# Optimization experiments

Hardware: AMD Instinct MI355X
Metric: run time of the kernel (lower is better)

Reference implementation:

```python
import jax, jax.numpy as jnp
import numpy as np

LR = 0.01
EPS = 1e-8
D, H, O, N = 1024, 256, 64, 1024


def _normalize(W, b):
    # L2 (Frobenius) normalize weights and biases, clamped at EPS
    wn = jnp.maximum(jnp.sqrt(jnp.sum(W * W)), EPS)
    bn = jnp.maximum(jnp.sqrt(jnp.sum(b * b)), EPS)
    return W / wn, b / bn


def _step(carry, xt):
    W1, b1, W2, b2, W3, b3 = carry
    x, t = xt
    # forward pass (3-layer sigmoid MLP, softmax over -a3 as in original)
    a1 = jax.nn.sigmoid(x @ W1 + b1)
    a2 = jax.nn.sigmoid(a1 @ W2 + b2)
    a3 = jax.nn.sigmoid(a2 @ W3 + b3)
    out = jax.nn.softmax(-a3)
    # manual backprop deltas
    d3 = (t - out) * a3 * (1.0 - a3)
    o2 = (W3 @ d3) * a2 * (1.0 - a2)
    o1 = (W2 @ o2) * a1 * (1.0 - a1)
    # SGD update (note: original subtracts the delta, matching .sub_)
    W3 = W3 - LR * jnp.outer(a2, d3)
    b3 = b3 - LR * d3
    W2 = W2 - LR * jnp.outer(a1, o2)
    b2 = b2 - LR * o2
    W1 = W1 - LR * jnp.outer(x, o1)
    b1 = b1 - LR * o1
    # L2 normalize each layer's weights/biases
    W1, b1 = _normalize(W1, b1)
    W2, b2 = _normalize(W2, b2)
    W3, b3 = _normalize(W3, b3)
    return (W1, b1, W2, b2, W3, b3), None


def setup_inputs() -> dict:
    key = jax.random.key(0)
    k = jax.random.split(key, 5)
    return {
        "training_data": jax.random.normal(k[0], (N, D), jnp.float32),
        "training_targets": jax.random.uniform(k[1], (N, O), dtype=jnp.float32),
        "weights1": jax.random.normal(k[2], (D, H), jnp.float32) * 0.01,
        "biases1": jnp.zeros((H,), jnp.float32),
        "weights2": jax.random.normal(k[3], (H, H), jnp.float32) * 0.01,
        "biases2": jnp.zeros((H,), jnp.float32),
        "weights3": jax.random.normal(k[4], (H, O), jnp.float32) * 0.01,
        "biases3": jnp.zeros((O,), jnp.float32),
    }


def reference(training_data, training_targets, weights1, biases1, weights2, biases2, weights3, biases3):
    carry0 = (weights1, biases1, weights2, biases2, weights3, biases3)
    carry, _ = jax.lax.scan(_step, carry0, (training_data, training_targets))
    W1, b1, W2, b2, W3, b3 = carry
    return (W1, W2, W3)
```

## Files before the change

kernel.cpp:

```cpp
#include <hip/hip_runtime.h>
#include <math.h>


#define LRC  0.01f
#define EPSV 1e-8f

typedef float f32x8 __attribute__((ext_vector_type(8)));

#define SMEM_FLOATS 36384
#define SMEM_BYTES  (SMEM_FLOATS * 4)

#define ROWS16(OP)                                                            \
  OP(0) OP(1) OP(2) OP(3) OP(4) OP(5) OP(6) OP(7)                             \
  OP(8) OP(9) OP(10) OP(11) OP(12) OP(13) OP(14) OP(15)

__device__ __forceinline__ float hsum8(f32x8 v) {
  return ((v.s0 + v.s1) + (v.s2 + v.s3)) + ((v.s4 + v.s5) + (v.s6 + v.s7));
}

template <int CTRL>
__device__ __forceinline__ float dpp_add(float v) {
  const int s = __builtin_amdgcn_update_dpp(0, __builtin_bit_cast(int, v),
                                            CTRL, 0xf, 0xf, true);
  return v + __builtin_bit_cast(float, s);
}

__device__ __forceinline__ float dpp_allred64(float v) {
  v = dpp_add<0x111>(v);
  v = dpp_add<0x112>(v);
  v = dpp_add<0x114>(v);
  v = dpp_add<0x118>(v);
  v = dpp_add<0x142>(v);
  v = dpp_add<0x143>(v);
  return __builtin_bit_cast(float,
      __builtin_amdgcn_readlane(__builtin_bit_cast(int, v), 63));
}

__device__ __forceinline__ float wave_allred(float v) {
#pragma unroll
  for (int off = 32; off > 0; off >>= 1) v += __shfl_xor(v, off);
  return v;
}

#define FMA16(c, a, b)                                                        \
  c[0][0] += a.x * b.x; c[0][1] += a.x * b.y; c[0][2] += a.x * b.z; c[0][3] += a.x * b.w; \
  c[1][0] += a.y * b.x; c[1][1] += a.y * b.y; c[1][2] += a.y * b.z; c[1][3] += a.y * b.w; \
  c[2][0] += a.z * b.x; c[2][1] += a.z * b.y; c[2][2] += a.z * b.z; c[2][3] += a.z * b.w; \
  c[3][0] += a.w * b.x; c[3][1] += a.w * b.y; c[3][2] += a.w * b.z; c[3][3] += a.w * b.w;

__global__ __launch_bounds__(256) void k_gram(const float* __restrict__ X,
                                              float* __restrict__ G) {
  const int bi = blockIdx.y, bj = blockIdx.x;
  if (bj > bi) return;
  __shared__ float Xa[32][68];
  __shared__ float Xb[32][68];
  const int tid = threadIdx.x;
  const int tx = tid & 15, ty = tid >> 4;
  float c[4][4] = {};
  for (int k0 = 0; k0 < 1024; k0 += 32) {
    __syncthreads();
    {
      const int row = tid >> 2, kk = (tid & 3) * 8;
      const float* pa = X + (bi * 64 + row) * 1024 + k0 + kk;
      const float4 a0 = *(const float4*)pa;
      const float4 a1 = *(const float4*)(pa + 4);
      Xa[kk + 0][row] = a0.x; Xa[kk + 1][row] = a0.y;
      Xa[kk + 2][row] = a0.z; Xa[kk + 3][row] = a0.w;
      Xa[kk + 4][row] = a1.x; Xa[kk + 5][row] = a1.y;
      Xa[kk + 6][row] = a1.z; Xa[kk + 7][row] = a1.w;
      const float* pb = X + (bj * 64 + row) * 1024 + k0 + kk;
      const float4 b0 = *(const float4*)pb;
      const float4 b1 = *(const float4*)(pb + 4);
      Xb[kk + 0][row] = b0.x; Xb[kk + 1][row] = b0.y;
      Xb[kk + 2][row] = b0.z; Xb[kk + 3][row] = b0.w;
      Xb[kk + 4][row] = b1.x; Xb[kk + 5][row] = b1.y;
      Xb[kk + 6][row] = b1.z; Xb[kk + 7][row] = b1.w;
    }
    __syncthreads();
#pragma unroll
    for (int kk = 0; kk < 32; kk++) {
      const float4 a = *(const float4*)&Xa[kk][ty * 4];
      const float4 b = *(const float4*)&Xb[kk][tx * 4];
      FMA16(c, a, b)
    }
  }
#pragma unroll
  for (int ii = 0; ii < 4; ii++) {
    *(float4*)(G + (bi * 64 + ty * 4 + ii) * 1024 + bj * 64 + tx * 4) =
        make_float4(c[ii][0], c[ii][1], c[ii][2], c[ii][3]);
  }
}

__global__ __launch_bounds__(256) void k_z10(const float* __restrict__ X,
                                             const float* __restrict__ W1g,
                                             float* __restrict__ Z10) {
  const int bi = blockIdx.y, bj = blockIdx.x;
  __shared__ float At[32][68];
  __shared__ float Bt[32][68];
  const int tid = threadIdx.x;
  const int tx = tid & 15, ty = tid >> 4;
  float c[4][4] = {};
  for (int k0 = 0; k0 < 1024; k0 += 32) {
    __syncthreads();
    {
      const int row = tid >> 2, kk = (tid & 3) * 8;
      const float* pa = X + (bi * 64 + row) * 1024 + k0 + kk;
      const float4 a0 = *(const float4*)pa;
      const float4 a1 = *(const float4*)(pa + 4);
      At[kk + 0][row] = a0.x; At[kk + 1][row] = a0.y;
      At[kk + 2][row] = a0.z; At[kk + 3][row] = a0.w;
      At[kk + 4][row] = a1.x; At[kk + 5][row] = a1.y;
      At[kk + 6][row] = a1.z; At[kk + 7][row] = a1.w;
      const int kr = tid >> 3, j8 = (tid & 7) * 8;
      const float* pb = W1g + (k0 + kr) * 256 + bj * 64 + j8;
      *(float4*)&Bt[kr][j8]     = *(const float4*)pb;
      *(float4*)&Bt[kr][j8 + 4] = *(const float4*)(pb + 4);
    }
    __syncthreads();
#pragma unroll
    for (int kk = 0; kk < 32; kk++) {
      const float4 a = *(const float4*)&At[kk][ty * 4];
      const float4 b = *(const float4*)&Bt[kk][tx * 4];
      FMA16(c, a, b)
    }
  }
#pragma unroll
  for (int ii = 0; ii < 4; ii++) {
    *(float4*)(Z10 + (bi * 64 + ty * 4 + ii) * 256 + bj * 64 + tx * 4) =
        make_float4(c[ii][0], c[ii][1], c[ii][2], c[ii][3]);
  }
}

__global__ __launch_bounds__(256) void k_w1out(
    const float* __restrict__ X, const float* __restrict__ o1g,
    const float* __restrict__ cg, const float* __restrict__ W1g,
    const float* __restrict__ sclg, float* __restrict__ outW1) {
  const int bi = blockIdx.y, bj = blockIdx.x;
  __shared__ float At[32][68];
  __shared__ float Bt[32][68];
  const int tid = threadIdx.x;
  const int tx = tid & 15, ty = tid >> 4;
  float c[4][4] = {};
  for (int k0 = 0; k0 < 1024; k0 += 32) {
    __syncthreads();
    {
      const int kr = tid >> 3, m8 = (tid & 7) * 8;
      const float* pa = X + (k0 + kr) * 1024 + bi * 64 + m8;
      *(float4*)&At[kr][m8]     = *(const float4*)pa;
      *(float4*)&At[kr][m8 + 4] = *(const float4*)(pa + 4);
      const float cs = cg[k0 + kr];
      const float* pb = o1g + (k0 + kr) * 256 + bj * 64 + m8;
      float4 b0 = *(const float4*)pb;
      float4 b1 = *(const float4*)(pb + 4);
      b0.x *= cs; b0.y *= cs; b0.z *= cs; b0.w *= cs;
      b1.x *= cs; b1.y *= cs; b1.z *= cs; b1.w *= cs;
      *(float4*)&Bt[kr][m8]     = b0;
      *(float4*)&Bt[kr][m8 + 4] = b1;
    }
    __syncthreads();
#pragma unroll
    for (int kk = 0; kk < 32; kk++) {
      const float4 a = *(const float4*)&At[kk][ty * 4];
      const float4 b = *(const float4*)&Bt[kk][tx * 4];
      FMA16(c, a, b)
    }
  }
  const float s1f = sclg[0];
#pragma unroll
  for (int ii = 0; ii < 4; ii++) {
    const int row = bi * 64 + ty * 4 + ii;
    const float4 w = *(const float4*)(W1g + row * 256 + bj * 64 + tx * 4);
    *(float4*)(outW1 + row * 256 + bj * 64 + tx * 4) =
        make_float4(s1f * (w.x + c[ii][0]), s1f * (w.y + c[ii][1]),
                    s1f * (w.z + c[ii][2]), s1f * (w.w + c[ii][3]));
  }
}

__device__ __forceinline__ float block_reduce8(float v, float* tmp, int tid) {
  v = wave_allred(v);
  __syncthreads();
  if ((tid & 63) == 0) tmp[tid >> 6] = v;
  __syncthreads();
  float s = 0.f;
#pragma unroll
  for (int w = 0; w < 8; w++) s += tmp[w];
  __syncthreads();
  return s;
}

__global__ __launch_bounds__(512, 1) void k2_seq(
    const float* __restrict__ Tg, const float* __restrict__ W1g,
    const float* __restrict__ b1g, const float* __restrict__ W2g,
    const float* __restrict__ b2g, const float* __restrict__ W3g,
    const float* __restrict__ b3g, const float* __restrict__ G,
    const float* __restrict__ Z10, float* __restrict__ o1g,
    float* __restrict__ cg, float* __restrict__ sclg,
    float* __restrict__ outW2, float* __restrict__ outW3) {
  extern __shared__ float sm[];
  float* const zo   = sm;
  float* const Gb   = sm + 17408;
  float* const scr  = sm + 21504;
  float* const Tb   = sm + 29952;
  float* const a1v  = sm + 34048;
  float* const z1v  = sm + 34560;
  float* const z2v  = sm + 34816;
  float* const a2v  = sm + 35072;
  float* const o2v  = sm + 35328;
  float* const b1ps = sm + 35584;
  float* const b2ps = sm + 35840;
  float* const d3v  = sm + 36096;
  float* const b3ps = sm + 36160;
  float* const ch   = sm + 36224;
  float* const dpart= sm + 36288;
  float* const sca  = sm + 36336;
  float* const cpre = sm + 36352;

  const int tid = threadIdx.x;
  const int lane = tid & 63;
  const int w = tid >> 6;
  const int p = tid >> 5;
  const int q = tid & 31;

  f32x8 W2_0, W2_1, W2_2, W2_3, W2_4, W2_5, W2_6, W2_7,
        W2_8, W2_9, W2_10, W2_11, W2_12, W2_13, W2_14, W2_15;
  float W3x_0, W3x_1, W3x_2, W3x_3, W3x_4, W3x_5, W3x_6, W3x_7,
        W3x_8, W3x_9, W3x_10, W3x_11, W3x_12, W3x_13, W3x_14, W3x_15;
  float W3y_0, W3y_1, W3y_2, W3y_3, W3y_4, W3y_5, W3y_6, W3y_7,
        W3y_8, W3y_9, W3y_10, W3y_11, W3y_12, W3y_13, W3y_14, W3y_15;

#define INIT_ROW(i)                                                           \
  { const int row = p * 16 + i;                                               \
    W2_##i  = *(const f32x8*)(W2g + row * 256 + q * 8);                       \
    W3x_##i = W3g[row * 64 + q * 2];                                          \
    W3y_##i = W3g[row * 64 + q * 2 + 1]; }
  ROWS16(INIT_ROW)

  if (tid < 256) { b1ps[tid] = b1g[tid]; b2ps[tid] = b2g[tid]; }
  if (tid < 64) b3ps[tid] = b3g[tid];
  if (tid == 0) {
    sca[0] = 1.f; sca[1] = 1.f; sca[2] = 1.f; sca[3] = 1.f;
    sca[4] = 1.f; sca[5] = 1.f; sca[6] = 0.f; sca[7] = 0.f;
  }

  float acc1 = 0.f;
  for (int i = tid; i < 65536; i += 512) {
    const float4 v = ((const float4*)W1g)[i];
    acc1 += v.x * v.x + v.y * v.y + v.z * v.z + v.w * v.w;
  }
  const float n1init = block_reduce8(acc1, scr, tid);
  float acc2 = 0.f;
#define N2_ROW(i) { f32x8 t = W2_##i * W2_##i; acc2 += hsum8(t); }
  ROWS16(N2_ROW)
  const float n2init = block_reduce8(acc2, scr, tid);
  float acc3 = 0.f;
#define N3_ROW(i) acc3 += W3x_##i * W3x_##i + W3y_##i * W3y_##i;
  ROWS16(N3_ROW)
  const float n3init = block_reduce8(acc3, scr, tid);

  float s1 = 1.f, s2 = 1.f, s3 = 1.f;
  double n1d = (double)n1init;
  float n2 = n2init, n3 = n3init;
  __syncthreads();

  for (int b = 0; b < 16; b++) {
    const int bs = b * 64;
    {
      f32x8 pacc0 = {0.f, 0.f, 0.f, 0.f, 0.f, 0.f, 0.f, 0.f};
      f32x8 pacc1 = pacc0, pacc2 = pacc0, pacc3 = pacc0;
      for (int c0 = 0; c0 < bs; c0 += 32) {
        __syncthreads();
        if (tid < 32) cpre[tid] = cg[c0 + tid];
        {
          const int row = tid >> 3, k4 = (tid & 7) * 4;
          const float4 gv = *(const float4*)(G + (bs + row) * 1024 + c0 + k4);
          Gb[row * 33 + k4 + 0] = gv.x; Gb[row * 33 + k4 + 1] = gv.y;
          Gb[row * 33 + k4 + 2] = gv.z; Gb[row * 33 + k4 + 3] = gv.w;
        }
#pragma unroll
        for (int u = 0; u < 4; u++) {
          const int fi = tid + u * 512;
          ((float4*)scr)[fi] = ((const float4*)(o1g + c0 * 256))[fi];
        }
        __syncthreads();
#pragma unroll 2
        for (int ss = 0; ss < 32; ss++) {
          const float cs = cpre[ss];
          const f32x8 o8 = *(const f32x8*)(scr + ss * 256 + q * 8);
          pacc0 += (Gb[(p * 4 + 0) * 33 + ss] * cs) * o8;
          pacc1 += (Gb[(p * 4 + 1) * 33 + ss] * cs) * o8;
          pacc2 += (Gb[(p * 4 + 2) * 33 + ss] * cs) * o8;
          pacc3 += (Gb[(p * 4 + 3) * 33 + ss] * cs) * o8;
        }
      }
      __syncthreads();
#define ZSTORE(rr)                                                            \
      { const int row = p * 4 + rr;                                           \
        *(f32x8*)(zo + row * 272 + q * 8) =                                   \
            *(const f32x8*)(Z10 + (bs + row) * 256 + q * 8) + pacc##rr; }
      ZSTORE(0) ZSTORE(1) ZSTORE(2) ZSTORE(3)
#pragma unroll
      for (int u = 0; u < 2; u++) {
        const int fi = tid + u * 512;
        const int row = fi >> 4, c4 = fi & 15;
        *(float4*)(Gb + row * 64 + c4 * 4) =
            *(const float4*)(G + (bs + row) * 1024 + bs + c4 * 4);
      }
      ((float4*)Tb)[tid]       = ((const float4*)(Tg + bs * 64))[tid];
      ((float4*)Tb)[tid + 512] = ((const float4*)(Tg + bs * 64))[tid + 512];
      __syncthreads();
    }

    for (int l = 0; l < 64; l++) {
      const int t = bs + l;
      const int cur = (t & 1) * 256, prv = 256 - cur;
      const float s1c = sca[0], rb1c = sca[1], s2c = sca[2],
                  rb2c = sca[3], s3c = sca[4], rb3c = sca[5];

      if (t > 0) {
        const float cw2 = sca[6], cw3 = sca[7];
        const f32x8 o8s = cw2 * (*(const f32x8*)&o2v[q * 8]);
        const float d0s = cw3 * d3v[q * 2], d1s = cw3 * d3v[q * 2 + 1];
#define UPD_ROW(i)                                                            \
        { const float a1o = a1v[prv + p * 16 + i];                            \
          W2_##i += a1o * o8s;                                                \
          const float a2o = a2v[p * 16 + i];                                  \
          W3x_##i += a2o * d0s; W3y_##i += a2o * d1s; }
        ROWS16(UPD_ROW)
      }
      {
        const int jp = tid >> 2, quarter = tid & 3;
        float ax = 0.f, ay = 0.f;
        for (int lp = quarter; lp < l; lp += 4) {
          const float gcs = ch[lp] * Gb[l * 64 + lp];
          const float2 zr = *(const float2*)&zo[lp * 272 + 2 * jp];
          ax += gcs * zr.x; ay += gcs * zr.y;
        }
        ax = dpp_add<0xB1>(ax); ax = dpp_add<0x4E>(ax);
        ay = dpp_add<0xB1>(ay); ay = dpp_add<0x4E>(ay);
        const float2 zop = *(const float2*)&zo[l * 272 + 2 * jp];
        const float2 b1q = *(const float2*)&b1ps[2 * jp];
        const float z1u0 = zop.x + ax, z1u1 = zop.y + ay;
        const float a1x0 = 1.f / (1.f + expf(-(s1c * z1u0 + rb1c * b1q.x)));
        const float a1x1 = 1.f / (1.f + expf(-(s1c * z1u1 + rb1c * b1q.y)));
        if (quarter == 0) {
          *(float2*)&z1v[2 * jp] = make_float2(z1u0, z1u1);
          *(float2*)&a1v[cur + 2 * jp] = make_float2(a1x0, a1x1);
        }
        const float v3 = dpp_allred64(
            quarter == 0 ? a1x0 * a1x0 + a1x1 * a1x1 : 0.f);
        if (lane == 0) dpart[36 + w] = v3;
      }
      __syncthreads();
      {
        f32x8 acc = {0.f, 0.f, 0.f, 0.f, 0.f, 0.f, 0.f, 0.f};
#define B1_ROW(i) acc += a1v[cur + p * 16 + i] * W2_##i;
        ROWS16(B1_ROW)
        *(f32x8*)&scr[p * 264 + q * 8] = acc;
      }
      __syncthreads();
      if (tid < 256) {
        float s = 0.f;
#pragma unroll
        for (int pp = 0; pp < 16; pp++) s += scr[pp * 264 + tid];
        const float z2p = s2c * s;
        z2v[tid] = z2p;
        a2v[tid] = 1.f / (1.f + expf(-(z2p + rb2c * b2ps[tid])));
      }
      __syncthreads();
      {
        float c0a = 0.f, c1a = 0.f;
#define C1_ROW(i)                                                             \
        { const float a2x = a2v[p * 16 + i];                                  \
          c0a += a2x * W3x_##i; c1a += a2x * W3y_##i; }
        ROWS16(C1_ROW)
        scr[(q * 2 + 0) * 17 + p] = c0a;
        scr[(q * 2 + 1) * 17 + p] = c1a;
      }
      __syncthreads();
      if (tid < 64) {
        float s = 0.f;
#pragma unroll
        for (int pp = 0; pp < 16; pp++) s += scr[tid * 17 + pp];
        const float z3p = s3c * s;
        const float a3 = 1.f / (1.f + expf(-(z3p + rb3c * b3ps[tid])));
        const float e = expf(-a3);
        const float tot = dpp_allred64(e);
        const float outv = e / tot;
        const float d3 = (Tb[l * 64 + tid] - outv) * a3 * (1.f - a3);
        d3v[tid] = d3;
        const float b3n = rb3c * b3ps[tid] - LRC * d3;
        b3ps[tid] = b3n;
        const float v5 = dpp_allred64(z3p * d3);
        const float v7 = dpp_allred64(d3 * d3);
        const float v10 = dpp_allred64(b3n * b3n);
        if (tid == 0) { dpart[32] = v5; dpart[33] = v7; dpart[34] = v10; }
      }
      __syncthreads();
      {
        const float d0 = d3v[q * 2 + 0], d1 = d3v[q * 2 + 1];
#define E1_ROW(i) scr[(p * 16 + i) * 33 + q] = W3x_##i * d0 + W3y_##i * d1;
        ROWS16(E1_ROW)
      }
      __syncthreads();
      if (tid < 256) {
        float s = 0.f;
#pragma unroll
        for (int qq = 0; qq < 32; qq++) s += scr[tid * 33 + qq];
        const float a2x = a2v[tid];
        const float o2 = s3c * s * a2x * (1.f - a2x);
        o2v[tid] = o2;
        const float b2n = rb2c * b2ps[tid] - LRC * o2;
        b2ps[tid] = b2n;
        const float v2 = dpp_allred64(z2v[tid] * o2);
        const float v4 = dpp_allred64(o2 * o2);
        const float v6 = dpp_allred64(a2x * a2x);
        const float v9 = dpp_allred64(b2n * b2n);
        if ((tid & 63) == 0) {
          dpart[16 + w] = v2; dpart[20 + w] = v4;
          dpart[24 + w] = v6; dpart[28 + w] = v9;
        }
      }
      __syncthreads();
      {
        const f32x8 ov8 = *(const f32x8*)&o2v[q * 8];
#define F1_ROW(i)                                                             \
        { f32x8 tmp = W2_##i * ov8; scr[(p * 16 + i) * 33 + q] = hsum8(tmp); }
        ROWS16(F1_ROW)
      }
      if (w == 7) {
        const float dts3 = ((dpart[36] + dpart[37]) + (dpart[38] + dpart[39]))
                         + ((dpart[40] + dpart[41]) + (dpart[42] + dpart[43]));
        const float dts2 = (dpart[16] + dpart[17]) + (dpart[18] + dpart[19]);
        const float dts4 = (dpart[20] + dpart[21]) + (dpart[22] + dpart[23]);
        const float dts6 = (dpart[24] + dpart[25]) + (dpart[26] + dpart[27]);
        const float dts9 = (dpart[28] + dpart[29]) + (dpart[30] + dpart[31]);
        const float dts5 = dpart[32], dts7 = dpart[33], dts10 = dpart[34];
        const float n2p = n2 - 2.f * LRC * dts2 + LRC * LRC * dts3 * dts4;
        const float r2s = 1.f / fmaxf(sqrtf(n2p), EPSV);
        n2 = n2p * r2s * r2s;
        const float cw2n = -LRC / s2;
        s2 = s2 * r2s;
        const float n3p = n3 - 2.f * LRC * dts5 + LRC * LRC * dts6 * dts7;
        const float r3s = 1.f / fmaxf(sqrtf(n3p), EPSV);
        n3 = n3p * r3s * r3s;
        const float cw3n = -LRC / s3;
        s3 = s3 * r3s;
        if (lane == 0) {
          sca[2] = s2;
          sca[3] = 1.f / fmaxf(sqrtf(dts9), EPSV);
          sca[4] = s3;
          sca[5] = 1.f / fmaxf(sqrtf(dts10), EPSV);
          sca[6] = cw2n;
          sca[7] = cw3n;
        }
      }
      __syncthreads();
      if (tid < 256) {
        float s = 0.f;
#pragma unroll
        for (int qq = 0; qq < 32; qq++) s += scr[tid * 33 + qq];
        const float a1x = a1v[cur + tid];
        const float o1x = s2c * s * a1x * (1.f - a1x);
        zo[l * 272 + tid] = o1x;
        const float b1n = rb1c * b1ps[tid] - LRC * o1x;
        b1ps[tid] = b1n;
        const float v0 = dpp_allred64(z1v[tid] * o1x);
        const float v1 = dpp_allred64(o1x * o1x);
        const float v8 = dpp_allred64(b1n * b1n);
        if ((tid & 63) == 0) {
          dpart[0 + w] = v0; dpart[4 + w] = v1; dpart[12 + w] = v8;
        }
      }
      __syncthreads();
      if (tid < 64) {
        const float dts0 = (dpart[0] + dpart[1]) + (dpart[2] + dpart[3]);
        const float dts1 = (dpart[4] + dpart[5]) + (dpart[6] + dpart[7]);
        const float dts8 = (dpart[12] + dpart[13]) + (dpart[14] + dpart[15]);
        const float c1 = -LRC / s1;
        const double gtt = (double)Gb[l * 64 + l];
        n1d = n1d + 2.0 * (double)c1 * (double)dts0 +
              (double)c1 * (double)c1 * gtt * (double)dts1;
        const double w1n = (double)s1 * sqrt(n1d);
        s1 = (float)((double)s1 / fmax(w1n, (double)EPSV));
        if (tid == 0) {
          ch[l] = c1;
          sca[0] = s1;
          sca[1] = 1.f / fmaxf(sqrtf(dts8), EPSV);
        }
      }
      __syncthreads();
    }

    {
#pragma unroll
      for (int u = 0; u < 4; u++) {
        const int chunk = tid + u * 512;
        const int row = chunk >> 5, c8 = chunk & 31;
        *(f32x8*)(o1g + (bs + row) * 256 + c8 * 8) =
            *(const f32x8*)(zo + row * 272 + c8 * 8);
      }
      if (tid < 64) cg[bs + tid] = ch[tid];
    }
  }

  {
    const float cw2 = sca[6], cw3 = sca[7];
    const float s2f = sca[2], s3f = sca[4];
    const f32x8 o8s = cw2 * (*(const f32x8*)&o2v[q * 8]);
    const float d0s = cw3 * d3v[q * 2], d1s = cw3 * d3v[q * 2 + 1];
#define FIN_ROW(i)                                                            \
    { const float a1o = a1v[256 + p * 16 + i];          \
      W2_##i += a1o * o8s;                                                    \
      const float a2o = a2v[p * 16 + i];                                      \
      W3x_##i += a2o * d0s; W3y_##i += a2o * d1s;                             \
      const int row = p * 16 + i;                                             \
      *(f32x8*)(outW2 + row * 256 + q * 8) = s2f * W2_##i;                    \
      outW3[row * 64 + q * 2]     = s3f * W3x_##i;                            \
      outW3[row * 64 + q * 2 + 1] = s3f * W3y_##i; }
    ROWS16(FIN_ROW)
    if (tid == 0) sclg[0] = sca[0];
  }
}

extern "C" void kernel_launch(void* const* d_in, const int* in_sizes, int n_in,
                              void* d_out, int out_size, void* d_ws,
                              size_t ws_size, hipStream_t stream) {
  (void)in_sizes; (void)n_in; (void)out_size; (void)ws_size;
  const float* X   = (const float*)d_in[0];
  const float* Tg  = (const float*)d_in[1];
  const float* W1g = (const float*)d_in[2];
  const float* b1g = (const float*)d_in[3];
  const float* W2g = (const float*)d_in[4];
  const float* b2g = (const float*)d_in[5];
  const float* W3g = (const float*)d_in[6];
  const float* b3g = (const float*)d_in[7];
  float* out = (float*)d_out;
  float* ws  = (float*)d_ws;

  float* G    = ws;
  float* Z10  = G + 1048576;
  float* o1g  = Z10 + 262144;
  float* cg   = o1g + 262144;
  float* sclg = cg + 1024;

  (void)hipFuncSetAttribute((const void*)k2_seq,
                            hipFuncAttributeMaxDynamicSharedMemorySize,
                            SMEM_BYTES);

  k_gram<<<dim3(16, 16), 256, 0, stream>>>(X, G);
  k_z10<<<dim3(4, 16), 256, 0, stream>>>(X, W1g, Z10);
  k2_seq<<<dim3(1), dim3(512), SMEM_BYTES, stream>>>(
      Tg, W1g, b1g, W2g, b2g, W3g, b3g, G, Z10, o1g, cg, sclg,
      out + 262144, out + 327680);
  k_w1out<<<dim3(4, 16), 256, 0, stream>>>(X, o1g, cg, W1g, sclg, out);
}
```

Baseline: 8.963 ms.

## Replicate scalar normalization chain per thread and cut per-step barriers

Drops the shared-memory scalar broadcast. Every thread now recomputes the norm/scale recurrence from partial dot products at the start of the next step, so the single-thread scalar stages and their barriers go away. The W3·d3 and W2·o2 row reductions now use an in-register DPP transpose tree instead of a shared-memory scratch round trip. The layer-3 softmax is computed by all waves, and b3 and the partial sums are double-buffered to avoid races. The aim is fewer __syncthreads per sequential step, at the cost of redundant scalar math in every thread and more register pressure.

```diff
diff --git a/kernel.cpp b/kernel.cpp
--- a/kernel.cpp
+++ b/kernel.cpp
@@ -7,7 +7,7 @@
 
 typedef float f32x8 __attribute__((ext_vector_type(8)));
 
-#define SMEM_FLOATS 36384
+#define SMEM_FLOATS 36456
 #define SMEM_BYTES  (SMEM_FLOATS * 4)
 
 #define ROWS16(OP)                                                            \
@@ -19,12 +19,14 @@
 }
 
 template <int CTRL>
+__device__ __forceinline__ float dpp_mov(float x) {
+  return __builtin_bit_cast(float, __builtin_amdgcn_update_dpp(
+      0, __builtin_bit_cast(int, x), CTRL, 0xf, 0xf, true));
+}
+template <int CTRL>
 __device__ __forceinline__ float dpp_add(float v) {
-  const int s = __builtin_amdgcn_update_dpp(0, __builtin_bit_cast(int, v),
-                                            CTRL, 0xf, 0xf, true);
-  return v + __builtin_bit_cast(float, s);
-}
-
+  return v + dpp_mov<CTRL>(v);
+}
 __device__ __forceinline__ float dpp_allred64(float v) {
   v = dpp_add<0x111>(v);
   v = dpp_add<0x112>(v);
@@ -35,12 +37,37 @@
   return __builtin_bit_cast(float,
       __builtin_amdgcn_readlane(__builtin_bit_cast(int, v), 63));
 }
+__device__ __forceinline__ float dpp_xor4(float x, bool hi) {
+  const float up = dpp_mov<0x104>(x);
+  const float dn = dpp_mov<0x114>(x);
+  return hi ? dn : up;
+}
+__device__ __forceinline__ float dpp_xor8(float x, bool hi) {
+  const float up = dpp_mov<0x108>(x);
+  const float dn = dpp_mov<0x118>(x);
+  return hi ? dn : up;
+}
 
 __device__ __forceinline__ float wave_allred(float v) {
 #pragma unroll
   for (int off = 32; off > 0; off >>= 1) v += __shfl_xor(v, off);
   return v;
 }
+
+#define TSTAGE(XEXPR, BITVAL, N2)                                             \
+  { _Pragma("unroll")                                                         \
+    for (int s = 0; s < N2; s++) {                                            \
+      const float aa = v[2 * s], bb = v[2 * s + 1];                           \
+      const float snd = (BITVAL) ? aa : bb;                                   \
+      const float kp = (BITVAL) ? bb : aa;                                    \
+      v[s] = kp + (XEXPR);                                                    \
+    } }
+#define TREE16()                                                              \
+  TSTAGE(dpp_mov<0xB1>(snd), bt1, 8)                                          \
+  TSTAGE(dpp_mov<0x4E>(snd), bt2, 4)                                          \
+  TSTAGE(dpp_xor4(snd, bt4), bt4, 2)                                          \
+  TSTAGE(dpp_xor8(snd, bt8), bt8, 1)                                          \
+  v[0] += __shfl_xor(v[0], 16);
 
 #define FMA16(c, a, b)                                                        \
   c[0][0] += a.x * b.x; c[0][1] += a.x * b.y; c[0][2] += a.x * b.z; c[0][3] += a.x * b.w; \
@@ -210,16 +237,18 @@
   float* const b2ps = sm + 35840;
   float* const d3v  = sm + 36096;
   float* const b3ps = sm + 36160;
-  float* const ch   = sm + 36224;
-  float* const dpart= sm + 36288;
-  float* const sca  = sm + 36336;
-  float* const cpre = sm + 36352;
+  float* const ch   = sm + 36288;
+  float* const dpart= sm + 36352;
+  float* const cpre = sm + 36424;
 
   const int tid = threadIdx.x;
   const int lane = tid & 63;
   const int w = tid >> 6;
   const int p = tid >> 5;
   const int q = tid & 31;
+  const int gl = lane & 31;
+  const bool bt1 = (lane & 1), bt2 = (lane & 2), bt4 = (lane & 4),
+             bt8 = (lane & 8);
 
   f32x8 W2_0, W2_1, W2_2, W2_3, W2_4, W2_5, W2_6, W2_7,
         W2_8, W2_9, W2_10, W2_11, W2_12, W2_13, W2_14, W2_15;
@@ -237,10 +266,6 @@
 
   if (tid < 256) { b1ps[tid] = b1g[tid]; b2ps[tid] = b2g[tid]; }
   if (tid < 64) b3ps[tid] = b3g[tid];
-  if (tid == 0) {
-    sca[0] = 1.f; sca[1] = 1.f; sca[2] = 1.f; sca[3] = 1.f;
-    sca[4] = 1.f; sca[5] = 1.f; sca[6] = 0.f; sca[7] = 0.f;
-  }
 
   float acc1 = 0.f;
   for (int i = tid; i < 65536; i += 512) {
@@ -258,9 +283,60 @@
   const float n3init = block_reduce8(acc3, scr, tid);
 
   float s1 = 1.f, s2 = 1.f, s3 = 1.f;
+  float rb1 = 1.f, rb2 = 1.f, rb3 = 1.f;
+  float c1r = 0.f, cw2r = 0.f, cw3r = 0.f;
   double n1d = (double)n1init;
   float n2 = n2init, n3 = n3init;
   __syncthreads();
+
+  auto run_chain = [&](const int lidx, const int pv3) {
+    const float4 qa0 = *(const float4*)&dpart[0];
+    const float4 qa1 = *(const float4*)&dpart[4];
+    const float4 qb0 = *(const float4*)&dpart[8];
+    const float4 qb1 = *(const float4*)&dpart[12];
+    const float4 qc0 = *(const float4*)&dpart[16];
+    const float4 qc1 = *(const float4*)&dpart[20];
+    const float4 qd0 = *(const float4*)&dpart[24];
+    const float4 qd1 = *(const float4*)&dpart[28];
+    const float4 qe0 = *(const float4*)&dpart[32];
+    const float4 qe1 = *(const float4*)&dpart[36];
+    const float4 qf0 = *(const float4*)&dpart[40];
+    const float4 qf1 = *(const float4*)&dpart[44];
+    const float4 qg0 = *(const float4*)&dpart[48 + pv3];
+    const float4 qg1 = *(const float4*)&dpart[52 + pv3];
+    const float4 qh  = *(const float4*)&dpart[64];
+    const float4 qi  = *(const float4*)&dpart[68];
+#define SUM8(x0, x1) (((x0.x + x0.y) + (x0.z + x0.w)) +                       \
+                      ((x1.x + x1.y) + (x1.z + x1.w)))
+    const float dts0 = SUM8(qa0, qa1);
+    const float dts1 = SUM8(qb0, qb1);
+    const float dts8 = SUM8(qc0, qc1);
+    const float dts2 = SUM8(qd0, qd1);
+    const float dts4 = SUM8(qe0, qe1);
+    const float dts9 = SUM8(qf0, qf1);
+    const float dts3 = SUM8(qg0, qg1);
+    const float dts5 = qh.x, dts7 = qh.y, dts10 = qh.z;
+    const float dts6 = (qi.x + qi.y) + (qi.z + qi.w);
+    const float c1 = -LRC / s1;
+    c1r = c1; cw2r = -LRC / s2; cw3r = -LRC / s3;
+    const double gtt = (double)Gb[lidx * 65];
+    n1d = n1d + 2.0 * (double)c1 * (double)dts0 +
+          (double)c1 * (double)c1 * gtt * (double)dts1;
+    const double w1n = (double)s1 * sqrt(n1d);
+    s1 = (float)((double)s1 / fmax(w1n, (double)EPSV));
+    rb1 = 1.f / fmaxf(sqrtf(dts8), EPSV);
+    const float n2p = n2 - 2.f * LRC * dts2 + LRC * LRC * dts3 * dts4;
+    const float r2s = 1.f / fmaxf(sqrtf(n2p), EPSV);
+    n2 = n2p * r2s * r2s;
+    s2 = s2 * r2s;
+    rb2 = 1.f / fmaxf(sqrtf(dts9), EPSV);
+    const float n3p = n3 - 2.f * LRC * dts5 + LRC * LRC * dts6 * dts7;
+    const float r3s = 1.f / fmaxf(sqrtf(n3p), EPSV);
+    n3 = n3p * r3s * r3s;
+    s3 = s3 * r3s;
+    rb3 = 1.f / fmaxf(sqrtf(dts10), EPSV);
+    if (tid == 0) ch[lidx] = c1;
+  };
 
   for (int b = 0; b < 16; b++) {
     const int bs = b * 64;
@@ -313,13 +389,11 @@
     for (int l = 0; l < 64; l++) {
       const int t = bs + l;
       const int cur = (t & 1) * 256, prv = 256 - cur;
-      const float s1c = sca[0], rb1c = sca[1], s2c = sca[2],
-                  rb2c = sca[3], s3c = sca[4], rb3c = sca[5];
-
+
+      if (l > 0) run_chain(l - 1, ((t - 1) & 1) * 8);
       if (t > 0) {
-        const float cw2 = sca[6], cw3 = sca[7];
-        const f32x8 o8s = cw2 * (*(const f32x8*)&o2v[q * 8]);
-        const float d0s = cw3 * d3v[q * 2], d1s = cw3 * d3v[q * 2 + 1];
+        const f32x8 o8s = cw2r * (*(const f32x8*)&o2v[q * 8]);
+        const float d0s = cw3r * d3v[q * 2], d1s = cw3r * d3v[q * 2 + 1];
 #define UPD_ROW(i)                                                            \
         { const float a1o = a1v[prv + p * 16 + i];                            \
           W2_##i += a1o * o8s;                                                \
@@ -330,9 +404,14 @@
       {
         const int jp = tid >> 2, quarter = tid & 3;
         float ax = 0.f, ay = 0.f;
-        for (int lp = quarter; lp < l; lp += 4) {
+        for (int lp = quarter; lp < l - 1; lp += 4) {
           const float gcs = ch[lp] * Gb[l * 64 + lp];
           const float2 zr = *(const float2*)&zo[lp * 272 + 2 * jp];
+          ax += gcs * zr.x; ay += gcs * zr.y;
+        }
+        if (l > 0 && ((l - 1) & 3) == quarter) {
+          const float gcs = c1r * Gb[l * 64 + (l - 1)];
+          const float2 zr = *(const float2*)&zo[(l - 1) * 272 + 2 * jp];
           ax += gcs * zr.x; ay += gcs * zr.y;
         }
         ax = dpp_add<0xB1>(ax); ax = dpp_add<0x4E>(ax);
@@ -340,17 +419,18 @@
         const float2 zop = *(const float2*)&zo[l * 272 + 2 * jp];
         const float2 b1q = *(const float2*)&b1ps[2 * jp];
         const float z1u0 = zop.x + ax, z1u1 = zop.y + ay;
-        const float a1x0 = 1.f / (1.f + expf(-(s1c * z1u0 + rb1c * b1q.x)));
-        const float a1x1 = 1.f / (1.f + expf(-(s1c * z1u1 + rb1c * b1q.y)));
+        const float a1x0 = 1.f / (1.f + expf(-(s1 * z1u0 + rb1 * b1q.x)));
+        const float a1x1 = 1.f / (1.f + expf(-(s1 * z1u1 + rb1 * b1q.y)));
         if (quarter == 0) {
           *(float2*)&z1v[2 * jp] = make_float2(z1u0, z1u1);
           *(float2*)&a1v[cur + 2 * jp] = make_float2(a1x0, a1x1);
         }
         const float v3 = dpp_allred64(
             quarter == 0 ? a1x0 * a1x0 + a1x1 * a1x1 : 0.f);
-        if (lane == 0) dpart[36 + w] = v3;
-      }
-      __syncthreads();
+        if (lane == 0) dpart[48 + (t & 1) * 8 + w] = v3;
+      }
+      __syncthreads();
+
       {
         f32x8 acc = {0.f, 0.f, 0.f, 0.f, 0.f, 0.f, 0.f, 0.f};
 #define B1_ROW(i) acc += a1v[cur + p * 16 + i] * W2_##i;
@@ -358,138 +438,108 @@
         *(f32x8*)&scr[p * 264 + q * 8] = acc;
       }
       __syncthreads();
+
       if (tid < 256) {
         float s = 0.f;
 #pragma unroll
         for (int pp = 0; pp < 16; pp++) s += scr[pp * 264 + tid];
-        const float z2p = s2c * s;
+        const float z2p = s2 * s;
         z2v[tid] = z2p;
-        a2v[tid] = 1.f / (1.f + expf(-(z2p + rb2c * b2ps[tid])));
-      }
-      __syncthreads();
+        const float a2x = 1.f / (1.f + expf(-(z2p + rb2 * b2ps[tid])));
+        a2v[tid] = a2x;
+        const float v6w = dpp_allred64(a2x * a2x);
+        if ((tid & 63) == 0) dpart[68 + (tid >> 6)] = v6w;
+      }
+      __syncthreads();
+
       {
         float c0a = 0.f, c1a = 0.f;
 #define C1_ROW(i)                                                             \
         { const float a2x = a2v[p * 16 + i];                                  \
           c0a += a2x * W3x_##i; c1a += a2x * W3y_##i; }
         ROWS16(C1_ROW)
-        scr[(q * 2 + 0) * 17 + p] = c0a;
-        scr[(q * 2 + 1) * 17 + p] = c1a;
-      }
-      __syncthreads();
-      if (tid < 64) {
-        float s = 0.f;
-#pragma unroll
-        for (int pp = 0; pp < 16; pp++) s += scr[tid * 17 + pp];
-        const float z3p = s3c * s;
-        const float a3 = 1.f / (1.f + expf(-(z3p + rb3c * b3ps[tid])));
-        const float e = expf(-a3);
-        const float tot = dpp_allred64(e);
-        const float outv = e / tot;
-        const float d3 = (Tb[l * 64 + tid] - outv) * a3 * (1.f - a3);
-        d3v[tid] = d3;
-        const float b3n = rb3c * b3ps[tid] - LRC * d3;
-        b3ps[tid] = b3n;
-        const float v5 = dpp_allred64(z3p * d3);
-        const float v7 = dpp_allred64(d3 * d3);
-        const float v10 = dpp_allred64(b3n * b3n);
-        if (tid == 0) { dpart[32] = v5; dpart[33] = v7; dpart[34] = v10; }
-      }
-      __syncthreads();
+        *(float2*)&scr[p * 130 + 2 * q] = make_float2(c0a, c1a);
+      }
+      __syncthreads();
+
       {
-        const float d0 = d3v[q * 2 + 0], d1 = d3v[q * 2 + 1];
-#define E1_ROW(i) scr[(p * 16 + i) * 33 + q] = W3x_##i * d0 + W3y_##i * d1;
-        ROWS16(E1_ROW)
-      }
-      __syncthreads();
-      if (tid < 256) {
-        float s = 0.f;
-#pragma unroll
-        for (int qq = 0; qq < 32; qq++) s += scr[tid * 33 + qq];
-        const float a2x = a2v[tid];
-        const float o2 = s3c * s * a2x * (1.f - a2x);
-        o2v[tid] = o2;
-        const float b2n = rb2c * b2ps[tid] - LRC * o2;
-        b2ps[tid] = b2n;
-        const float v2 = dpp_allred64(z2v[tid] * o2);
-        const float v4 = dpp_allred64(o2 * o2);
-        const float v6 = dpp_allred64(a2x * a2x);
-        const float v9 = dpp_allred64(b2n * b2n);
-        if ((tid & 63) == 0) {
-          dpart[16 + w] = v2; dpart[20 + w] = v4;
-          dpart[24 + w] = v6; dpart[28 + w] = v9;
-        }
-      }
-      __syncthreads();
+        float z30 = 0.f, z31 = 0.f;
+#pragma unroll
+        for (int pp = 0; pp < 16; pp++) {
+          const float2 zz = *(const float2*)&scr[pp * 130 + 2 * q];
+          z30 += zz.x; z31 += zz.y;
+        }
+        const float z3p0 = s3 * z30, z3p1 = s3 * z31;
+        const int pbR = (t & 1) * 64, pbW = 64 - pbR;
+        const float b3o0 = b3ps[pbR + 2 * q], b3o1 = b3ps[pbR + 2 * q + 1];
+        const float a30 = 1.f / (1.f + expf(-(z3p0 + rb3 * b3o0)));
+        const float a31 = 1.f / (1.f + expf(-(z3p1 + rb3 * b3o1)));
+        const float e0 = expf(-a30), e1 = expf(-a31);
+        const float tot2 = dpp_allred64(e0 + e1);
+        const float out0 = (2.f * e0) / tot2, out1 = (2.f * e1) / tot2;
+        const float2 tb = *(const float2*)&Tb[l * 64 + 2 * q];
+        const float d30 = (tb.x - out0) * a30 * (1.f - a30);
+        const float d31 = (tb.y - out1) * a31 * (1.f - a31);
+        const float b3n0 = rb3 * b3o0 - LRC * d30;
+        const float b3n1 = rb3 * b3o1 - LRC * d31;
+        if (tid < 32) {
+          d3v[2 * q] = d30; d3v[2 * q + 1] = d31;
+          b3ps[pbW + 2 * q] = b3n0; b3ps[pbW + 2 * q + 1] = b3n1;
+        }
+        const float v5w = dpp_allred64(z3p0 * d30 + z3p1 * d31);
+        const float v7w = dpp_allred64(d30 * d30 + d31 * d31);
+        const float v10w = dpp_allred64(b3n0 * b3n0 + b3n1 * b3n1);
+        if (tid == 0) {
+          dpart[64] = 0.5f * v5w; dpart[65] = 0.5f * v7w;
+          dpart[66] = 0.5f * v10w;
+        }
+        float v[16];
+#define CE_ROW(i) v[i] = W3x_##i * d30 + W3y_##i * d31;
+        ROWS16(CE_ROW)
+        TREE16()
+        const int r = p * 16 + (gl & 15);
+        const float a2x = a2v[r];
+        const float o2x = s3 * v[0] * a2x * (1.f - a2x);
+        const float z2x = z2v[r];
+        const float b2o = b2ps[r];
+        const float b2n = rb2 * b2o - LRC * o2x;
+        if (gl < 16) { o2v[r] = o2x; b2ps[r] = b2n; }
+        const bool own = gl < 16;
+        const float v2w = dpp_allred64(own ? z2x * o2x : 0.f);
+        const float v4w = dpp_allred64(own ? o2x * o2x : 0.f);
+        const float v9w = dpp_allred64(own ? b2n * b2n : 0.f);
+        if (lane == 0) {
+          dpart[24 + w] = v2w; dpart[32 + w] = v4w; dpart[40 + w] = v9w;
+        }
+      }
+      __syncthreads();
+
       {
         const f32x8 ov8 = *(const f32x8*)&o2v[q * 8];
-#define F1_ROW(i)                                                             \
-        { f32x8 tmp = W2_##i * ov8; scr[(p * 16 + i) * 33 + q] = hsum8(tmp); }
-        ROWS16(F1_ROW)
-      }
-      if (w == 7) {
-        const float dts3 = ((dpart[36] + dpart[37]) + (dpart[38] + dpart[39]))
-                         + ((dpart[40] + dpart[41]) + (dpart[42] + dpart[43]));
-        const float dts2 = (dpart[16] + dpart[17]) + (dpart[18] + dpart[19]);
-        const float dts4 = (dpart[20] + dpart[21]) + (dpart[22] + dpart[23]);
-        const float dts6 = (dpart[24] + dpart[25]) + (dpart[26] + dpart[27]);
-        const float dts9 = (dpart[28] + dpart[29]) + (dpart[30] + dpart[31]);
-        const float dts5 = dpart[32], dts7 = dpart[33], dts10 = dpart[34];
-        const float n2p = n2 - 2.f * LRC * dts2 + LRC * LRC * dts3 * dts4;
-        const float r2s = 1.f / fmaxf(sqrtf(n2p), EPSV);
-        n2 = n2p * r2s * r2s;
-        const float cw2n = -LRC / s2;
-        s2 = s2 * r2s;
-        const float n3p = n3 - 2.f * LRC * dts5 + LRC * LRC * dts6 * dts7;
-        const float r3s = 1.f / fmaxf(sqrtf(n3p), EPSV);
-        n3 = n3p * r3s * r3s;
-        const float cw3n = -LRC / s3;
-        s3 = s3 * r3s;
+        float v[16];
+#define F_ROW(i) { f32x8 tq = W2_##i * ov8; v[i] = hsum8(tq); }
+        ROWS16(F_ROW)
+        TREE16()
+        const int r = p * 16 + (gl & 15);
+        const float a1x = a1v[cur + r];
+        const float o1x = s2 * v[0] * a1x * (1.f - a1x);
+        const float b1o = b1ps[r];
+        const float b1n = rb1 * b1o - LRC * o1x;
+        const float z1x = z1v[r];
+        if (gl < 16) { zo[l * 272 + r] = o1x; b1ps[r] = b1n; }
+        const bool own = gl < 16;
+        const float v0w = dpp_allred64(own ? z1x * o1x : 0.f);
+        const float v1w = dpp_allred64(own ? o1x * o1x : 0.f);
+        const float v8w = dpp_allred64(own ? b1n * b1n : 0.f);
         if (lane == 0) {
-          sca[2] = s2;
-          sca[3] = 1.f / fmaxf(sqrtf(dts9), EPSV);
-          sca[4] = s3;
-          sca[5] = 1.f / fmaxf(sqrtf(dts10), EPSV);
-          sca[6] = cw2n;
-          sca[7] = cw3n;
-        }
-      }
-      __syncthreads();
-      if (tid < 256) {
-        float s = 0.f;
-#pragma unroll
-        for (int qq = 0; qq < 32; qq++) s += scr[tid * 33 + qq];
-        const float a1x = a1v[cur + tid];
-        const float o1x = s2c * s * a1x * (1.f - a1x);
-        zo[l * 272 + tid] = o1x;
-        const float b1n = rb1c * b1ps[tid] - LRC * o1x;
-        b1ps[tid] = b1n;
-        const float v0 = dpp_allred64(z1v[tid] * o1x);
-        const float v1 = dpp_allred64(o1x * o1x);
-        const float v8 = dpp_allred64(b1n * b1n);
-        if ((tid & 63) == 0) {
-          dpart[0 + w] = v0; dpart[4 + w] = v1; dpart[12 + w] = v8;
-        }
-      }
-      __syncthreads();
-      if (tid < 64) {
-        const float dts0 = (dpart[0] + dpart[1]) + (dpart[2] + dpart[3]);
-        const float dts1 = (dpart[4] + dpart[5]) + (dpart[6] + dpart[7]);
-        const float dts8 = (dpart[12] + dpart[13]) + (dpart[14] + dpart[15]);
-        const float c1 = -LRC / s1;
-        const double gtt = (double)Gb[l * 64 + l];
-        n1d = n1d + 2.0 * (double)c1 * (double)dts0 +
-              (double)c1 * (double)c1 * gtt * (double)dts1;
-        const double w1n = (double)s1 * sqrt(n1d);
-        s1 = (float)((double)s1 / fmax(w1n, (double)EPSV));
-        if (tid == 0) {
-          ch[l] = c1;
-          sca[0] = s1;
-          sca[1] = 1.f / fmaxf(sqrtf(dts8), EPSV);
-        }
-      }
-      __syncthreads();
-    }
+          dpart[0 + w] = v0w; dpart[8 + w] = v1w; dpart[16 + w] = v8w;
+        }
+      }
+      __syncthreads();
+    }
+
+    run_chain(63, ((bs + 63) & 1) * 8);
+    __syncthreads();
 
     {
 #pragma unroll
@@ -504,21 +554,19 @@
   }
 
   {
-    const float cw2 = sca[6], cw3 = sca[7];
-    const float s2f = sca[2], s3f = sca[4];
-    const f32x8 o8s = cw2 * (*(const f32x8*)&o2v[q * 8]);
-    const float d0s = cw3 * d3v[q * 2], d1s = cw3 * d3v[q * 2 + 1];
+    const f32x8 o8s = cw2r * (*(const f32x8*)&o2v[q * 8]);
+    const float d0s = cw3r * d3v[q * 2], d1s = cw3r * d3v[q * 2 + 1];
 #define FIN_ROW(i)                                                            \
     { const float a1o = a1v[256 + p * 16 + i];          \
       W2_##i += a1o * o8s;                                                    \
       const float a2o = a2v[p * 16 + i];                                      \
       W3x_##i += a2o * d0s; W3y_##i += a2o * d1s;                             \
       const int row = p * 16 + i;                                             \
-      *(f32x8*)(outW2 + row * 256 + q * 8) = s2f * W2_##i;                    \
-      outW3[row * 64 + q * 2]     = s3f * W3x_##i;                            \
-      outW3[row * 64 + q * 2 + 1] = s3f * W3y_##i; }
+      *(f32x8*)(outW2 + row * 256 + q * 8) = s2 * W2_##i;                     \
+      outW3[row * 64 + q * 2]     = s3 * W3x_##i;                             \
+      outW3[row * 64 + q * 2 + 1] = s3 * W3y_##i; }
     ROWS16(FIN_ROW)
-    if (tid == 0) sclg[0] = sca[0];
+    if (tid == 0) sclg[0] = s1;
   }
 }
 
```

Result: slower. 10.56 ms (+17.8%).

## Defer W2 rank-1 update off critical path and cut per-step barriers

Applied to the files above, without the earlier changes.

The lagged W2 outer-product update now runs in otherwise idle warps during the layer-2/layer-3 reductions. The forward z2 is corrected algebraically with a dot product of the current and previous a1 vectors. The o2 and o1 row reductions are folded into the same phase as their scratch writes, each wave reducing its own rows behind a waitcnt fence, which removes two block-wide barriers per sample. The risk is extra reductions, a changed summation order and a fragile reliance on wave-local ordering of LDS writes.

```diff
diff --git a/kernel.cpp b/kernel.cpp
--- a/kernel.cpp
+++ b/kernel.cpp
@@ -7,7 +7,7 @@
 
 typedef float f32x8 __attribute__((ext_vector_type(8)));
 
-#define SMEM_FLOATS 36384
+#define SMEM_FLOATS 36400
 #define SMEM_BYTES  (SMEM_FLOATS * 4)
 
 #define ROWS16(OP)                                                            \
@@ -40,6 +40,12 @@
 #pragma unroll
   for (int off = 32; off > 0; off >>= 1) v += __shfl_xor(v, off);
   return v;
+}
+
+__device__ __forceinline__ void wave_fence() {
+  __builtin_amdgcn_sched_barrier(0);
+  asm volatile("s_waitcnt lgkmcnt(0)" ::: "memory");
+  __builtin_amdgcn_sched_barrier(0);
 }
 
 #define FMA16(c, a, b)                                                        \
@@ -212,14 +218,15 @@
   float* const b3ps = sm + 36160;
   float* const ch   = sm + 36224;
   float* const dpart= sm + 36288;
-  float* const sca  = sm + 36336;
-  float* const cpre = sm + 36352;
+  float* const sca  = sm + 36360;
+  float* const cpre = sm + 36368;
 
   const int tid = threadIdx.x;
   const int lane = tid & 63;
   const int w = tid >> 6;
   const int p = tid >> 5;
   const int q = tid & 31;
+  const int rown = 32 * w + (lane & 31);
 
   f32x8 W2_0, W2_1, W2_2, W2_3, W2_4, W2_5, W2_6, W2_7,
         W2_8, W2_9, W2_10, W2_11, W2_12, W2_13, W2_14, W2_15;
@@ -235,7 +242,11 @@
     W3y_##i = W3g[row * 64 + q * 2 + 1]; }
   ROWS16(INIT_ROW)
 
-  if (tid < 256) { b1ps[tid] = b1g[tid]; b2ps[tid] = b2g[tid]; }
+  if (tid < 256) {
+    b1ps[tid] = b1g[tid]; b2ps[tid] = b2g[tid];
+    o2v[tid] = 0.f;
+    a1v[tid] = 0.f; a1v[256 + tid] = 0.f;
+  }
   if (tid < 64) b3ps[tid] = b3g[tid];
   if (tid == 0) {
     sca[0] = 1.f; sca[1] = 1.f; sca[2] = 1.f; sca[3] = 1.f;
@@ -313,19 +324,27 @@
     for (int l = 0; l < 64; l++) {
       const int t = bs + l;
       const int cur = (t & 1) * 256, prv = 256 - cur;
-      const float s1c = sca[0], rb1c = sca[1], s2c = sca[2],
-                  rb2c = sca[3], s3c = sca[4], rb3c = sca[5];
+      const float s1c = sca[0], rb1c = sca[1], s2c = sca[2], rb2c = sca[3],
+                  s3c = sca[4], rb3c = sca[5], cw2c = sca[6], cw3c = sca[7];
+
+#define W2_UPD()                                                              \
+      { const f32x8 o8s = cw2c * (*(const f32x8*)&o2v[q * 8]);                \
+        const float* apv = &a1v[prv + p * 16];                                \
+        W2_0  += apv[0]  * o8s; W2_1  += apv[1]  * o8s;                       \
+        W2_2  += apv[2]  * o8s; W2_3  += apv[3]  * o8s;                       \
+        W2_4  += apv[4]  * o8s; W2_5  += apv[5]  * o8s;                       \
+        W2_6  += apv[6]  * o8s; W2_7  += apv[7]  * o8s;                       \
+        W2_8  += apv[8]  * o8s; W2_9  += apv[9]  * o8s;                       \
+        W2_10 += apv[10] * o8s; W2_11 += apv[11] * o8s;                       \
+        W2_12 += apv[12] * o8s; W2_13 += apv[13] * o8s;                       \
+        W2_14 += apv[14] * o8s; W2_15 += apv[15] * o8s; }
 
       if (t > 0) {
-        const float cw2 = sca[6], cw3 = sca[7];
-        const f32x8 o8s = cw2 * (*(const f32x8*)&o2v[q * 8]);
-        const float d0s = cw3 * d3v[q * 2], d1s = cw3 * d3v[q * 2 + 1];
-#define UPD_ROW(i)                                                            \
-        { const float a1o = a1v[prv + p * 16 + i];                            \
-          W2_##i += a1o * o8s;                                                \
-          const float a2o = a2v[p * 16 + i];                                  \
+        const float d0s = cw3c * d3v[q * 2], d1s = cw3c * d3v[q * 2 + 1];
+#define UPD3_ROW(i)                                                           \
+        { const float a2o = a2v[p * 16 + i];                                  \
           W3x_##i += a2o * d0s; W3y_##i += a2o * d1s; }
-        ROWS16(UPD_ROW)
+        ROWS16(UPD3_ROW)
       }
       {
         const int jp = tid >> 2, quarter = tid & 3;
@@ -339,6 +358,7 @@
         ay = dpp_add<0xB1>(ay); ay = dpp_add<0x4E>(ay);
         const float2 zop = *(const float2*)&zo[l * 272 + 2 * jp];
         const float2 b1q = *(const float2*)&b1ps[2 * jp];
+        const float2 ap  = *(const float2*)&a1v[prv + 2 * jp];
         const float z1u0 = zop.x + ax, z1u1 = zop.y + ay;
         const float a1x0 = 1.f / (1.f + expf(-(s1c * z1u0 + rb1c * b1q.x)));
         const float a1x1 = 1.f / (1.f + expf(-(s1c * z1u1 + rb1c * b1q.y)));
@@ -348,9 +368,12 @@
         }
         const float v3 = dpp_allred64(
             quarter == 0 ? a1x0 * a1x0 + a1x1 * a1x1 : 0.f);
-        if (lane == 0) dpart[36 + w] = v3;
-      }
-      __syncthreads();
+        const float vad = dpp_allred64(
+            quarter == 0 ? a1x0 * ap.x + a1x1 * ap.y : 0.f);
+        if (lane == 0) { dpart[48 + w] = v3; dpart[56 + w] = vad; }
+      }
+      __syncthreads();
+
       {
         f32x8 acc = {0.f, 0.f, 0.f, 0.f, 0.f, 0.f, 0.f, 0.f};
 #define B1_ROW(i) acc += a1v[cur + p * 16 + i] * W2_##i;
@@ -358,15 +381,24 @@
         *(f32x8*)&scr[p * 264 + q * 8] = acc;
       }
       __syncthreads();
+
       if (tid < 256) {
         float s = 0.f;
 #pragma unroll
         for (int pp = 0; pp < 16; pp++) s += scr[pp * 264 + tid];
-        const float z2p = s2c * s;
+        const float adot = ((dpart[56] + dpart[57]) + (dpart[58] + dpart[59]))
+                         + ((dpart[60] + dpart[61]) + (dpart[62] + dpart[63]));
+        const float z2p = s2c * (s + cw2c * adot * o2v[tid]);
         z2v[tid] = z2p;
-        a2v[tid] = 1.f / (1.f + expf(-(z2p + rb2c * b2ps[tid])));
-      }
-      __syncthreads();
+        const float a2x = 1.f / (1.f + expf(-(z2p + rb2c * b2ps[tid])));
+        a2v[tid] = a2x;
+        const float v6 = dpp_allred64(a2x * a2x);
+        if ((tid & 63) == 0) dpart[64 + (tid >> 6)] = v6;
+      } else if (t > 0) {
+        W2_UPD()
+      }
+      __syncthreads();
+
       {
         float c0a = 0.f, c1a = 0.f;
 #define C1_ROW(i)                                                             \
@@ -377,64 +409,104 @@
         scr[(q * 2 + 1) * 17 + p] = c1a;
       }
       __syncthreads();
-      if (tid < 64) {
+
+      if (w == 7) {
         float s = 0.f;
 #pragma unroll
-        for (int pp = 0; pp < 16; pp++) s += scr[tid * 17 + pp];
+        for (int pp = 0; pp < 16; pp++) s += scr[lane * 17 + pp];
         const float z3p = s3c * s;
-        const float a3 = 1.f / (1.f + expf(-(z3p + rb3c * b3ps[tid])));
+        const float a3 = 1.f / (1.f + expf(-(z3p + rb3c * b3ps[lane])));
         const float e = expf(-a3);
         const float tot = dpp_allred64(e);
         const float outv = e / tot;
-        const float d3 = (Tb[l * 64 + tid] - outv) * a3 * (1.f - a3);
-        d3v[tid] = d3;
-        const float b3n = rb3c * b3ps[tid] - LRC * d3;
-        b3ps[tid] = b3n;
+        const float d3 = (Tb[l * 64 + lane] - outv) * a3 * (1.f - a3);
+        d3v[lane] = d3;
+        const float b3n = rb3c * b3ps[lane] - LRC * d3;
+        b3ps[lane] = b3n;
         const float v5 = dpp_allred64(z3p * d3);
         const float v7 = dpp_allred64(d3 * d3);
         const float v10 = dpp_allred64(b3n * b3n);
-        if (tid == 0) { dpart[32] = v5; dpart[33] = v7; dpart[34] = v10; }
-      }
-      __syncthreads();
+        if (lane == 0) { dpart[68] = v5; dpart[69] = v7; dpart[70] = v10; }
+      } else if (w < 4 && t > 0) {
+        W2_UPD()
+      }
+      __syncthreads();
+
       {
         const float d0 = d3v[q * 2 + 0], d1 = d3v[q * 2 + 1];
 #define E1_ROW(i) scr[(p * 16 + i) * 33 + q] = W3x_##i * d0 + W3y_##i * d1;
         ROWS16(E1_ROW)
-      }
-      __syncthreads();
-      if (tid < 256) {
+        wave_fence();
         float s = 0.f;
 #pragma unroll
-        for (int qq = 0; qq < 32; qq++) s += scr[tid * 33 + qq];
-        const float a2x = a2v[tid];
-        const float o2 = s3c * s * a2x * (1.f - a2x);
-        o2v[tid] = o2;
-        const float b2n = rb2c * b2ps[tid] - LRC * o2;
-        b2ps[tid] = b2n;
-        const float v2 = dpp_allred64(z2v[tid] * o2);
-        const float v4 = dpp_allred64(o2 * o2);
-        const float v6 = dpp_allred64(a2x * a2x);
-        const float v9 = dpp_allred64(b2n * b2n);
-        if ((tid & 63) == 0) {
-          dpart[16 + w] = v2; dpart[20 + w] = v4;
-          dpart[24 + w] = v6; dpart[28 + w] = v9;
-        }
-      }
-      __syncthreads();
+        for (int qq = 0; qq < 32; qq++) s += scr[rown * 33 + qq];
+        const float a2x = a2v[rown];
+        const float o2x = s3c * s * a2x * (1.f - a2x);
+        const float b2n = rb2c * b2ps[rown] - LRC * o2x;
+        const bool own = (lane & 32) == 0;
+        if (own) { o2v[rown] = o2x; b2ps[rown] = b2n; }
+        const float v2 = dpp_allred64(own ? z2v[rown] * o2x : 0.f);
+        const float v4 = dpp_allred64(own ? o2x * o2x : 0.f);
+        const float v9 = dpp_allred64(own ? b2n * b2n : 0.f);
+        if (lane == 0) {
+          dpart[24 + w] = v2; dpart[32 + w] = v4; dpart[40 + w] = v9;
+        }
+      }
+      __syncthreads();
+
       {
         const f32x8 ov8 = *(const f32x8*)&o2v[q * 8];
-#define F1_ROW(i)                                                             \
-        { f32x8 tmp = W2_##i * ov8; scr[(p * 16 + i) * 33 + q] = hsum8(tmp); }
-        ROWS16(F1_ROW)
-      }
-      if (w == 7) {
-        const float dts3 = ((dpart[36] + dpart[37]) + (dpart[38] + dpart[39]))
-                         + ((dpart[40] + dpart[41]) + (dpart[42] + dpart[43]));
-        const float dts2 = (dpart[16] + dpart[17]) + (dpart[18] + dpart[19]);
-        const float dts4 = (dpart[20] + dpart[21]) + (dpart[22] + dpart[23]);
-        const float dts6 = (dpart[24] + dpart[25]) + (dpart[26] + dpart[27]);
-        const float dts9 = (dpart[28] + dpart[29]) + (dpart[30] + dpart[31]);
-        const float dts5 = dpart[32], dts7 = dpart[33], dts10 = dpart[34];
+#define F_ROW(i)                                                              \
+        { f32x8 tq = W2_##i * ov8; scr[(p * 16 + i) * 33 + q] = hsum8(tq); }
+        ROWS16(F_ROW)
+        wave_fence();
+        float s = 0.f;
+#pragma unroll
+        for (int qq = 0; qq < 32; qq++) s += scr[rown * 33 + qq];
+        const float a1x = a1v[cur + rown];
+        const float o1x = s2c * s * a1x * (1.f - a1x);
+        const float b1n = rb1c * b1ps[rown] - LRC * o1x;
+        const float z1x = z1v[rown];
+        const bool own = (lane & 32) == 0;
+        if (own) { zo[l * 272 + rown] = o1x; b1ps[rown] = b1n; }
+        const float v0 = dpp_allred64(own ? z1x * o1x : 0.f);
+        const float v1 = dpp_allred64(own ? o1x * o1x : 0.f);
+        const float v8 = dpp_allred64(own ? b1n * b1n : 0.f);
+        if (lane == 0) {
+          dpart[0 + w] = v0; dpart[8 + w] = v1; dpart[16 + w] = v8;
+        }
+      }
+      __syncthreads();
+
+      if (w == 0) {
+        const float dts0 = ((dpart[0] + dpart[1]) + (dpart[2] + dpart[3]))
+                         + ((dpart[4] + dpart[5]) + (dpart[6] + dpart[7]));
+        const float dts1 = ((dpart[8] + dpart[9]) + (dpart[10] + dpart[11]))
+                         + ((dpart[12] + dpart[13]) + (dpart[14] + dpart[15]));
+        const float dts8 = ((dpart[16] + dpart[17]) + (dpart[18] + dpart[19]))
+                         + ((dpart[20] + dpart[21]) + (dpart[22] + dpart[23]));
+        const float c1 = -LRC / s1;
+        const double gtt = (double)Gb[l * 65];
+        n1d = n1d + 2.0 * (double)c1 * (double)dts0 +
+              (double)c1 * (double)c1 * gtt * (double)dts1;
+        const double w1n = (double)s1 * sqrt(n1d);
+        s1 = (float)((double)s1 / fmax(w1n, (double)EPSV));
+        if (lane == 0) {
+          ch[l] = c1;
+          sca[0] = s1;
+          sca[1] = 1.f / fmaxf(sqrtf(dts8), EPSV);
+        }
+      } else if (w == 7) {
+        const float dts2 = ((dpart[24] + dpart[25]) + (dpart[26] + dpart[27]))
+                         + ((dpart[28] + dpart[29]) + (dpart[30] + dpart[31]));
+        const float dts4 = ((dpart[32] + dpart[33]) + (dpart[34] + dpart[35]))
+                         + ((dpart[36] + dpart[37]) + (dpart[38] + dpart[39]));
+        const float dts9 = ((dpart[40] + dpart[41]) + (dpart[42] + dpart[43]))
+                         + ((dpart[44] + dpart[45]) + (dpart[46] + dpart[47]));
+        const float dts3 = ((dpart[48] + dpart[49]) + (dpart[50] + dpart[51]))
+                         + ((dpart[52] + dpart[53]) + (dpart[54] + dpart[55]));
+        const float dts6 = (dpart[64] + dpart[65]) + (dpart[66] + dpart[67]);
+        const float dts5 = dpart[68], dts7 = dpart[69], dts10 = dpart[70];
         const float n2p = n2 - 2.f * LRC * dts2 + LRC * LRC * dts3 * dts4;
         const float r2s = 1.f / fmaxf(sqrtf(n2p), EPSV);
         n2 = n2p * r2s * r2s;
@@ -455,40 +527,6 @@
         }
       }
       __syncthreads();
-      if (tid < 256) {
-        float s = 0.f;
-#pragma unroll
-        for (int qq = 0; qq < 32; qq++) s += scr[tid * 33 + qq];
-        const float a1x = a1v[cur + tid];
-        const float o1x = s2c * s * a1x * (1.f - a1x);
-        zo[l * 272 + tid] = o1x;
-        const float b1n = rb1c * b1ps[tid] - LRC * o1x;
-        b1ps[tid] = b1n;
-        const float v0 = dpp_allred64(z1v[tid] * o1x);
-        const float v1 = dpp_allred64(o1x * o1x);
-        const float v8 = dpp_allred64(b1n * b1n);
-        if ((tid & 63) == 0) {
-          dpart[0 + w] = v0; dpart[4 + w] = v1; dpart[12 + w] = v8;
-        }
-      }
-      __syncthreads();
-      if (tid < 64) {
-        const float dts0 = (dpart[0] + dpart[1]) + (dpart[2] + dpart[3]);
-        const float dts1 = (dpart[4] + dpart[5]) + (dpart[6] + dpart[7]);
-        const float dts8 = (dpart[12] + dpart[13]) + (dpart[14] + dpart[15]);
-        const float c1 = -LRC / s1;
-        const double gtt = (double)Gb[l * 64 + l];
-        n1d = n1d + 2.0 * (double)c1 * (double)dts0 +
-              (double)c1 * (double)c1 * gtt * (double)dts1;
-        const double w1n = (double)s1 * sqrt(n1d);
-        s1 = (float)((double)s1 / fmax(w1n, (double)EPSV));
-        if (tid == 0) {
-          ch[l] = c1;
-          sca[0] = s1;
-          sca[1] = 1.f / fmaxf(sqrtf(dts8), EPSV);
-        }
-      }
-      __syncthreads();
     }
 
     {
@@ -504,10 +542,10 @@
   }
 
   {
-    const float cw2 = sca[6], cw3 = sca[7];
+    const float cw2f = sca[6], cw3f = sca[7];
     const float s2f = sca[2], s3f = sca[4];
-    const f32x8 o8s = cw2 * (*(const f32x8*)&o2v[q * 8]);
-    const float d0s = cw3 * d3v[q * 2], d1s = cw3 * d3v[q * 2 + 1];
+    const f32x8 o8s = cw2f * (*(const f32x8*)&o2v[q * 8]);
+    const float d0s = cw3f * d3v[q * 2], d1s = cw3f * d3v[q * 2 + 1];
 #define FIN_ROW(i)                                                            \
     { const float a1o = a1v[256 + p * 16 + i];          \
       W2_##i += a1o * o8s;                                                    \
```

Result: faster. 8.657 ms (-3.4%).
